# Kernel optimization log

Measured on AMD Instinct MI355X. Metric: run time of the kernel, lower is better.

The kernel has to match this reference:

```python
import jax, jax.numpy as jnp
import numpy as np

B, N, D = 16, 96, 128
NUM_TOKENS, NUM_CLASSES = 14, 10
NUM_ROUNDS = 5


def setup_inputs() -> dict:
    key = jax.random.key(0)
    ks = jax.random.split(key, 8)
    def lin(k, fan_in, shape):
        return (jax.random.normal(k, shape, jnp.float32) / np.sqrt(fan_in)).astype(jnp.float32)
    return {
        "tok": jax.random.randint(ks[0], (B, N), 0, NUM_TOKENS),
        "A": jax.random.uniform(ks[1], (B, N, N), jnp.float32),
        "embed_W": jax.random.normal(ks[2], (NUM_TOKENS, D), jnp.float32),
        "W1": lin(ks[3], 2 * D, (2 * D, D)),   # msg_fc1, stored [in, out]
        "b1": jnp.zeros((D,), jnp.float32),
        "W2": lin(ks[4], D, (D, D)),           # msg_fc2
        "b2": jnp.zeros((D,), jnp.float32),
        "Wo1": lin(ks[5], D, (D, D)),          # out_fc1
        "bo1": jnp.zeros((D,), jnp.float32),
        "Wo2": lin(ks[6], D, (D, NUM_CLASSES)),  # out_fc2 (no bias)
        "alpha": 0, "tau": 1, "beta": 0, "hard": 0,
    }


def reference(tok, A, embed_W, W1, b1, W2, b2, Wo1, bo1, Wo2, alpha, tau, beta, hard):
    # tok: [B,N] int, A: [B,N,N]. Dropout in eval mode (identity).
    e = embed_W[tok]                      # [B,N,D] token embeddings
    centroids = embed_W[4:]               # [10,D]
    W1e, W1x = W1[:D], W1[D:]             # split of msg_fc1 over the concat [e_i ; x_j]
    e_proj = jnp.einsum('bid,de->bie', e, W1e)  # constant across rounds

    def head(x2d):  # out_fc2(relu(out_fc1(x)))
        return jnp.maximum(x2d @ Wo1 + bo1, 0.0) @ Wo2

    def discretize(x):
        logits = head(x.reshape(-1, D))
        # beta=0, hard=False: gumbel_softmax degenerates to tempered softmax
        a = jax.nn.softmax(logits / tau, axis=-1)
        return (a @ centroids).reshape(x.shape)

    x = e
    for r in range(NUM_ROUNDS):
        xj_proj = jnp.einsum('bjd,de->bje', x, W1x)
        # h[b,i,j] = relu(msg_fc1([e_i ; x_j])) without materializing the concat
        h = jnp.maximum(e_proj[:, :, None, :] + xj_proj[:, None, :, :] + b1, 0.0)  # [B,N,N,D]
        m = jnp.maximum(jnp.einsum('bijd,de->bije', h, W2) + b2, 0.0)
        agg = jnp.einsum('bji,bijd->bid', A, m)  # A^T masked sum over j
        x = x + agg
        if r < NUM_ROUNDS - 1:
            # resid=True, alpha=0 -> np.random.random() > 0 a.s. -> residual add
            x = x + discretize(x)
    out = head(x[:, 0, :])                                  # [B,10]
    x_all = head(x.reshape(-1, D)).reshape(B, N, NUM_CLASSES)  # [B,N,10]
    return out, x_all
```

## Files before the change

### kernel.cpp

```cpp
#include <hip/hip_runtime.h>
#include <hip/hip_bf16.h>
#include <math.h>

#define BB   16
#define NN   96
#define DD   128
#define NCLS 10
#define NTOK 14

typedef __attribute__((ext_vector_type(8))) short bf16x8;
typedef __attribute__((ext_vector_type(8))) unsigned short u16x8;
typedef __attribute__((ext_vector_type(4))) float f32x4;

__device__ __forceinline__ float scalar_as_float(int v) {
    if (v >= -1000000 && v <= 1000000) return (float)v;
    return __int_as_float(v);
}
__device__ __forceinline__ unsigned short f2bf(float f) {
    unsigned u = __float_as_uint(f);
    return (unsigned short)((u + 0x7FFFu + ((u >> 16) & 1u)) >> 16);
}
__device__ __forceinline__ unsigned short f2bf_fast(float f) {
    __hip_bfloat16 b = __float2bfloat16(f);
    return *reinterpret_cast<unsigned short*>(&b);
}
__device__ __forceinline__ float bf2f(unsigned short h) {
    return __uint_as_float(((unsigned)h) << 16);
}

#define MFMA(A, B, C) __builtin_amdgcn_mfma_f32_16x16x32_bf16(A, B, C, 0, 0, 0)

__device__ __forceinline__ int swz_bx() {
    const int bxr = blockIdx.x;
    return ((bxr & 7) << 6) | (bxr >> 3);
}

__global__ __launch_bounds__(256) void k_prep(
    const float* __restrict__ A, const float* __restrict__ embed_W,
    const float* __restrict__ W1, const float* __restrict__ b1,
    const float* __restrict__ W2, const float* __restrict__ b2,
    const float* __restrict__ Wo1,
    float* __restrict__ Mtab, float* __restrict__ t2tab, float* __restrict__ AT,
    unsigned short* __restrict__ w2hi, unsigned short* __restrict__ w1xb,
    unsigned short* __restrict__ wo1b)
{
    const int bx = blockIdx.x;
    const int t  = threadIdx.x;
    const float* W1x = W1 + DD * DD;

    if (bx < NTOK * NTOK) {
        const int ti = bx / NTOK, tj = bx % NTOK;
        const int d = t & 127, half = t >> 7;
        __shared__ float part[2][DD];
        __shared__ unsigned short hb[DD];
        {
            const float* erow  = embed_W + (half ? tj : ti) * DD;
            const float* wbase = half ? W1x : W1;
            float acc = 0.f;
#pragma unroll 8
            for (int k = 0; k < DD; ++k)
                acc = fmaf(erow[k], wbase[k * DD + d], acc);
            part[half][d] = acc;
        }
        __syncthreads();
        if (half == 0) {
            const float v = part[0][d] + b1[d];
            if (tj == 0) t2tab[ti * DD + d] = v;
            hb[d] = f2bf(fmaxf(v + part[1][d], 0.f));
        }
        __syncthreads();
        {
            float m = 0.f;
#pragma unroll 8
            for (int kk = 0; kk < 64; ++kk) {
                const int k = half * 64 + kk;
                m = fmaf(bf2f(hb[k]), bf2f(f2bf(W2[k * DD + d])), m);
            }
            part[half][d] = m;
        }
        __syncthreads();
        if (half == 0)
            Mtab[(ti * NTOK + tj) * DD + d] = fmaxf(part[0][d] + part[1][d] + b2[d], 0.f);
    } else if (bx < 212) {
        const int b = bx - 196;
        __shared__ float tile[NN][NN + 1];
        for (int idx = t; idx < NN * NN; idx += 256)
            tile[idx / NN][idx % NN] = A[b * NN * NN + idx];
        __syncthreads();
        for (int idx = t; idx < NN * NN; idx += 256) {
            const int i = idx / NN, j = idx % NN;
            AT[b * NN * NN + idx] = tile[j][i];
        }
    } else if (bx < 220) {
        const int dt = bx - 212;
        const int kc = t >> 6, ll = t & 63;
        const int base = ((dt * 4 + kc) * 64 + ll) * 8;
        const int c = dt * 16 + (ll & 15);
#pragma unroll
        for (int e = 0; e < 8; ++e)
            w2hi[base + e] = f2bf(W2[(kc * 32 + (ll >> 4) * 8 + e) * DD + c]);
    } else if (bx < 224) {
        const int base = (bx - 220) * 4096 + t * 16;
#pragma unroll
        for (int e = 0; e < 16; ++e) w1xb[base + e] = f2bf(W1x[base + e]);
    } else {
        const int base = (bx - 224) * 4096 + t * 16;
#pragma unroll
        for (int e = 0; e < 16; ++e) wo1b[base + e] = f2bf(Wo1[base + e]);
    }
}

__global__ __launch_bounds__(512, 4) void k_round0(
    const int* __restrict__ tok, const float* __restrict__ AT,
    const float* __restrict__ Mtab, const float* __restrict__ embed_W,
    const unsigned short* __restrict__ wo1b, const float* __restrict__ bo1,
    const float* __restrict__ Wo2, const unsigned short* __restrict__ w1xb,
    const int* __restrict__ tau_p,
    float* __restrict__ x, unsigned short* __restrict__ xj_out)
{
    const int bx = swz_bx();
    const int b  = bx >> 5;
    const int is = bx & 31;
    const int t  = threadIdx.x;
    const int w  = t >> 6;
    const int l  = t & 63;
    const int row0 = b * NN + is;

    __shared__ __align__(16) float mt[3][NTOK * DD];
    __shared__ float at3[3][NN];
    __shared__ int   tkj[NN];
    __shared__ float agg_s[3][DD];
    __shared__ float xn_s[3][DD];
    __shared__ float part_s[4][3][DD];

    const int ti0 = tok[row0], ti1 = tok[row0 + 32], ti2 = tok[row0 + 64];
    if (t < NN) {
        tkj[t]    = tok[b * NN + t];
        at3[0][t] = AT[row0 * NN + t];
        at3[1][t] = AT[(row0 + 32) * NN + t];
        at3[2][t] = AT[(row0 + 64) * NN + t];
    }
    for (int idx = t; idx < 3 * NTOK * DD; idx += 512) {
        const int u = idx / (NTOK * DD), rd = idx - u * (NTOK * DD);
        const int tiu = (u == 0) ? ti0 : ((u == 1) ? ti1 : ti2);
        mt[u][rd] = Mtab[tiu * NTOK * DD + rd];
    }
    __syncthreads();

    if (t < 192) {
        const int u = t >> 6, d2 = t & 63;
        const float2* mtu = (const float2*)mt[u];
        float2 acc = {0.f, 0.f};
#pragma unroll 4
        for (int j = 0; j < NN; ++j) {
            const float a = at3[u][j];
            const float2 m = mtu[tkj[j] * 64 + d2];
            acc.x = fmaf(a, m.x, acc.x);
            acc.y = fmaf(a, m.y, acc.y);
        }
        *(float2*)&agg_s[u][d2 * 2] = acc;
    }
    __syncthreads();

    float xr0 = 0.f, xr1 = 0.f;
    if (w < 3) {
        const int tk = (w == 0) ? ti0 : ((w == 1) ? ti1 : ti2);
        xr0 = embed_W[tk * DD + l]      + agg_s[w][l];
        xr1 = embed_W[tk * DD + l + 64] + agg_s[w][l + 64];
        xn_s[w][l]      = xr0;
        xn_s[w][l + 64] = xr1;
    }
    __syncthreads();

    {
        const int q = t >> 7, h = t & 127;
        float p0 = 0.f, p1 = 0.f, p2 = 0.f;
#pragma unroll
        for (int kk = 0; kk < 32; ++kk) {
            const int k = q * 32 + kk;
            const float wv = bf2f(wo1b[k * DD + h]);
            p0 = fmaf(xn_s[0][k], wv, p0);
            p1 = fmaf(xn_s[1][k], wv, p1);
            p2 = fmaf(xn_s[2][k], wv, p2);
        }
        part_s[q][0][h] = p0; part_s[q][1][h] = p1; part_s[q][2][h] = p2;
    }
    __syncthreads();

    if (w < 3) {
        const int row_u = row0 + 32 * w;
        const float hid0 = fmaxf(part_s[0][w][l] + part_s[1][w][l]
                               + part_s[2][w][l] + part_s[3][w][l] + bo1[l], 0.f);
        const float hid1 = fmaxf(part_s[0][w][l + 64] + part_s[1][w][l + 64]
                               + part_s[2][w][l + 64] + part_s[3][w][l + 64] + bo1[l + 64], 0.f);
        float lgp[NCLS];
#pragma unroll
        for (int c = 0; c < NCLS; ++c)
            lgp[c] = hid0 * Wo2[l * NCLS + c] + hid1 * Wo2[(l + 64) * NCLS + c];
#pragma unroll
        for (int s = 1; s < 64; s <<= 1) {
#pragma unroll
            for (int c = 0; c < NCLS; ++c) lgp[c] += __shfl_xor(lgp[c], s);
        }
        float mx = -1e30f;
#pragma unroll
        for (int c = 0; c < NCLS; ++c) mx = fmaxf(mx, lgp[c]);
        const float inv_tau = 1.f / scalar_as_float(tau_p[0]);
        float p[NCLS], den = 0.f;
#pragma unroll
        for (int c = 0; c < NCLS; ++c) { p[c] = expf((lgp[c] - mx) * inv_tau); den += p[c]; }
        const float invden = 1.f / den;
#pragma unroll
        for (int c = 0; c < NCLS; ++c) {
            const float pc = p[c] * invden;
            xr0 = fmaf(pc, embed_W[(4 + c) * DD + l], xr0);
            xr1 = fmaf(pc, embed_W[(4 + c) * DD + l + 64], xr1);
        }
        x[row_u * DD + l]      = xr0;
        x[row_u * DD + l + 64] = xr1;
        xn_s[w][l]      = xr0;
        xn_s[w][l + 64] = xr1;
    }
    __syncthreads();

    {
        const int q = t >> 7, h = t & 127;
        float p0 = 0.f, p1 = 0.f, p2 = 0.f;
#pragma unroll
        for (int kk = 0; kk < 32; ++kk) {
            const int k = q * 32 + kk;
            const float wv = bf2f(w1xb[k * DD + h]);
            p0 = fmaf(xn_s[0][k], wv, p0);
            p1 = fmaf(xn_s[1][k], wv, p1);
            p2 = fmaf(xn_s[2][k], wv, p2);
        }
        part_s[q][0][h] = p0; part_s[q][1][h] = p1; part_s[q][2][h] = p2;
    }
    __syncthreads();

    if (w < 3) {
        const int row_u = row0 + 32 * w;
        xj_out[row_u * DD + l] =
            f2bf_fast(part_s[0][w][l] + part_s[1][w][l] + part_s[2][w][l] + part_s[3][w][l]);
        xj_out[row_u * DD + l + 64] =
            f2bf_fast(part_s[0][w][l + 64] + part_s[1][w][l + 64]
                    + part_s[2][w][l + 64] + part_s[3][w][l + 64]);
    }
}

template<int FIN>
__global__ __launch_bounds__(512, 4) void k_round(
    const int* __restrict__ tok, const float* __restrict__ AT,
    const float* __restrict__ t2tab,
    const unsigned short* __restrict__ xj_in,
    const unsigned short* __restrict__ w2hi, const float* __restrict__ b2,
    const float* __restrict__ Wo1, const unsigned short* __restrict__ wo1b,
    const float* __restrict__ bo1, const float* __restrict__ Wo2,
    const float* __restrict__ embed_W, const unsigned short* __restrict__ w1xb,
    const int* __restrict__ tau_p,
    float* __restrict__ x, unsigned short* __restrict__ xj_out,
    float* __restrict__ out, float* __restrict__ x_all)
{
    const int bx = swz_bx();
    const int b  = bx >> 5;
    const int is = bx & 31;
    const int t  = threadIdx.x;
    const int w  = t >> 6;
    const int l  = t & 63;
    const int jg  = w >> 2;
    const int dg  = w & 3;
    const int jg3 = jg * 3;
    const int d0 = (t & 15) * 8;
    const int row0 = b * NN + is;

    __shared__ __align__(16) unsigned short hs[2][NN * DD];
    __shared__ float ac_s[3][NN];
    __shared__ float agg_part[3][2][DD];
    __shared__ float xn_s[3][DD];
    __shared__ float part_s[4][3][DD];

    const int tk0 = tok[row0], tk1 = tok[row0 + 32], tk2 = tok[row0 + 64];

    if (t < NN) {
        ac_s[0][t] = AT[row0 * NN + t];
        ac_s[1][t] = AT[(row0 + 32) * NN + t];
        ac_s[2][t] = AT[(row0 + 64) * NN + t];
    }
    float xr0 = 0.f, xr1 = 0.f;
    if (w < 3) {
        const int row_u = row0 + 32 * w;
        xr0 = x[row_u * DD + l];
        xr1 = x[row_u * DD + l + 64];
    }

    const bf16x8* WH = (const bf16x8*)w2hi;
    const int f0 = (dg * 4) * 64 + l;
    const int f1 = ((dg + 4) * 4) * 64 + l;
    bf16x8 bh00 = WH[f0],        bh10 = WH[f1];
    bf16x8 bh01 = WH[f0 + 64],   bh11 = WH[f1 + 64];
    bf16x8 bh02 = WH[f0 + 128],  bh12 = WH[f1 + 128];
    bf16x8 bh03 = WH[f0 + 192],  bh13 = WH[f1 + 192];
    asm volatile("" : "+v"(bh00), "+v"(bh01), "+v"(bh02), "+v"(bh03),
                      "+v"(bh10), "+v"(bh11), "+v"(bh12), "+v"(bh13));
    const float b2v0 = b2[dg * 16 + (l & 15)];
    const float b2v1 = b2[64 + dg * 16 + (l & 15)];
    const u16x8* xj8 = (const u16x8*)(xj_in + b * NN * DD);

    const u16x8 xva = xj8[t];
    const u16x8 xvb = xj8[t + 512];
    const u16x8 xvc = xj8[t + 1024];
    const int j_a = t >> 4, j_b = (t + 512) >> 4, j_c = (t + 1024) >> 4;

    auto STAGE = [&](int u, int p) {
        const int tk = (u == 0) ? tk0 : ((u == 1) ? tk1 : tk2);
        const float4 ea = *(const float4*)(t2tab + tk * DD + d0);
        const float4 eb = *(const float4*)(t2tab + tk * DD + d0 + 4);
        float v8[8];
        v8[0] = ea.x; v8[1] = ea.y; v8[2] = ea.z; v8[3] = ea.w;
        v8[4] = eb.x; v8[5] = eb.y; v8[6] = eb.z; v8[7] = eb.w;
        u16x8 hh;
#pragma unroll
        for (int e = 0; e < 8; ++e) hh[e] = f2bf_fast(fmaxf(bf2f(xva[e]) + v8[e], 0.f));
        *(u16x8*)&hs[p][(j_a * DD + d0) ^ ((j_a & 7) << 3)] = hh;
#pragma unroll
        for (int e = 0; e < 8; ++e) hh[e] = f2bf_fast(fmaxf(bf2f(xvb[e]) + v8[e], 0.f));
        *(u16x8*)&hs[p][(j_b * DD + d0) ^ ((j_b & 7) << 3)] = hh;
#pragma unroll
        for (int e = 0; e < 8; ++e) hh[e] = f2bf_fast(fmaxf(bf2f(xvc[e]) + v8[e], 0.f));
        *(u16x8*)&hs[p][(j_c * DD + d0) ^ ((j_c & 7) << 3)] = hh;
    };

    auto GEMM = [&](int u, int p) {
        float aggp0 = 0.f, aggp1 = 0.f;
        const unsigned short* hb = hs[p];
#pragma unroll
        for (int jj = 0; jj < 3; ++jj) {
            const int jt  = jg3 + jj;
            const int r16 = jt * 16 + (l & 15);
            const int ko  = (l >> 4) * 8;
            const int sw  = (r16 & 7) << 3;
            const bf16x8 a0 = *(const bf16x8*)&hb[(r16 * DD + ko     ) ^ sw];
            const bf16x8 a1 = *(const bf16x8*)&hb[(r16 * DD + ko + 32) ^ sw];
            const bf16x8 a2 = *(const bf16x8*)&hb[(r16 * DD + ko + 64) ^ sw];
            const bf16x8 a3 = *(const bf16x8*)&hb[(r16 * DD + ko + 96) ^ sw];
            f32x4 c0 = {0.f, 0.f, 0.f, 0.f}, c1 = {0.f, 0.f, 0.f, 0.f};
            c0 = MFMA(a0, bh00, c0);  c1 = MFMA(a0, bh10, c1);
            c0 = MFMA(a1, bh01, c0);  c1 = MFMA(a1, bh11, c1);
            c0 = MFMA(a2, bh02, c0);  c1 = MFMA(a2, bh12, c1);
            c0 = MFMA(a3, bh03, c0);  c1 = MFMA(a3, bh13, c1);
#pragma unroll
            for (int r = 0; r < 4; ++r) {
                const float a = ac_s[u][jt * 16 + (l >> 4) * 4 + r];
                aggp0 = fmaf(a, fmaxf(c0[r] + b2v0, 0.f), aggp0);
                aggp1 = fmaf(a, fmaxf(c1[r] + b2v1, 0.f), aggp1);
            }
        }
        aggp0 += __shfl_xor(aggp0, 16); aggp0 += __shfl_xor(aggp0, 32);
        aggp1 += __shfl_xor(aggp1, 16); aggp1 += __shfl_xor(aggp1, 32);
        if (l < 16) {
            agg_part[u][jg][dg * 16 + l]      = aggp0;
            agg_part[u][jg][64 + dg * 16 + l] = aggp1;
        }
    };

    STAGE(0, 0);
    __syncthreads();
    STAGE(1, 1);
    GEMM(0, 0);
    __syncthreads();
    STAGE(2, 0);
    GEMM(1, 1);
    __syncthreads();
    GEMM(2, 0);
    __syncthreads();

    if (w < 3) {
        xr0 += agg_part[w][0][l]      + agg_part[w][1][l];
        xr1 += agg_part[w][0][l + 64] + agg_part[w][1][l + 64];
        xn_s[w][l]      = xr0;
        xn_s[w][l + 64] = xr1;
    }
    __syncthreads();

    {
        const int q = t >> 7, h = t & 127;
        float p0 = 0.f, p1 = 0.f, p2 = 0.f;
#pragma unroll
        for (int kk = 0; kk < 32; ++kk) {
            const int k = q * 32 + kk;
            const float wv = FIN ? Wo1[k * DD + h] : bf2f(wo1b[k * DD + h]);
            p0 = fmaf(xn_s[0][k], wv, p0);
            p1 = fmaf(xn_s[1][k], wv, p1);
            p2 = fmaf(xn_s[2][k], wv, p2);
        }
        part_s[q][0][h] = p0; part_s[q][1][h] = p1; part_s[q][2][h] = p2;
    }
    __syncthreads();

    if (w < 3) {
        const int row_u = row0 + 32 * w;
        const float hid0 = fmaxf(part_s[0][w][l] + part_s[1][w][l]
                               + part_s[2][w][l] + part_s[3][w][l] + bo1[l], 0.f);
        const float hid1 = fmaxf(part_s[0][w][l + 64] + part_s[1][w][l + 64]
                               + part_s[2][w][l + 64] + part_s[3][w][l + 64] + bo1[l + 64], 0.f);
        float lgp[NCLS];
#pragma unroll
        for (int c = 0; c < NCLS; ++c)
            lgp[c] = hid0 * Wo2[l * NCLS + c] + hid1 * Wo2[(l + 64) * NCLS + c];
#pragma unroll
        for (int s = 1; s < 64; s <<= 1) {
#pragma unroll
            for (int c = 0; c < NCLS; ++c) lgp[c] += __shfl_xor(lgp[c], s);
        }
        if (FIN) {
#pragma unroll
            for (int c = 0; c < NCLS; ++c) {
                if (l == c) {
                    x_all[row_u * NCLS + c] = lgp[c];
                    if (is == 0 && w == 0) out[b * NCLS + c] = lgp[c];
                }
            }
        } else {
            float mx = -1e30f;
#pragma unroll
            for (int c = 0; c < NCLS; ++c) mx = fmaxf(mx, lgp[c]);
            const float inv_tau = 1.f / scalar_as_float(tau_p[0]);
            float p[NCLS], den = 0.f;
#pragma unroll
            for (int c = 0; c < NCLS; ++c) { p[c] = expf((lgp[c] - mx) * inv_tau); den += p[c]; }
            const float invden = 1.f / den;
#pragma unroll
            for (int c = 0; c < NCLS; ++c) {
                const float pc = p[c] * invden;
                xr0 = fmaf(pc, embed_W[(4 + c) * DD + l], xr0);
                xr1 = fmaf(pc, embed_W[(4 + c) * DD + l + 64], xr1);
            }
            x[row_u * DD + l]      = xr0;
            x[row_u * DD + l + 64] = xr1;
            xn_s[w][l]      = xr0;
            xn_s[w][l + 64] = xr1;
        }
    }
    if (FIN) return;
    __syncthreads();

    {
        const int q = t >> 7, h = t & 127;
        float p0 = 0.f, p1 = 0.f, p2 = 0.f;
#pragma unroll
        for (int kk = 0; kk < 32; ++kk) {
            const int k = q * 32 + kk;
            const float wv = bf2f(w1xb[k * DD + h]);
            p0 = fmaf(xn_s[0][k], wv, p0);
            p1 = fmaf(xn_s[1][k], wv, p1);
            p2 = fmaf(xn_s[2][k], wv, p2);
        }
        part_s[q][0][h] = p0; part_s[q][1][h] = p1; part_s[q][2][h] = p2;
    }
    __syncthreads();

    if (w < 3) {
        const int row_u = row0 + 32 * w;
        xj_out[row_u * DD + l] =
            f2bf_fast(part_s[0][w][l] + part_s[1][w][l] + part_s[2][w][l] + part_s[3][w][l]);
        xj_out[row_u * DD + l + 64] =
            f2bf_fast(part_s[0][w][l + 64] + part_s[1][w][l + 64]
                    + part_s[2][w][l + 64] + part_s[3][w][l + 64]);
    }
}

extern "C" void kernel_launch(void* const* d_in, const int* in_sizes, int n_in,
                              void* d_out, int out_size, void* d_ws, size_t ws_size,
                              hipStream_t stream)
{
    (void)in_sizes; (void)n_in; (void)out_size; (void)ws_size;
    const int*   tok     = (const int*)d_in[0];
    const float* Aab     = (const float*)d_in[1];
    const float* embed_W = (const float*)d_in[2];
    const float* W1      = (const float*)d_in[3];
    const float* b1      = (const float*)d_in[4];
    const float* W2      = (const float*)d_in[5];
    const float* b2      = (const float*)d_in[6];
    const float* Wo1     = (const float*)d_in[7];
    const float* bo1     = (const float*)d_in[8];
    const float* Wo2     = (const float*)d_in[9];
    const int*   tau_p   = (const int*)d_in[11];

    float* out   = (float*)d_out;
    float* x_all = out + BB * NCLS;

    float* ws     = (float*)d_ws;
    float* x      = ws;
    float* ATr    = ws + BB * NN * DD;
    float* Mtab   = ATr + BB * NN * NN;
    float* t2tab  = Mtab + NTOK * NTOK * DD;
    unsigned short* xjA  = (unsigned short*)(t2tab + NTOK * DD);
    unsigned short* xjB  = xjA + BB * NN * DD;
    unsigned short* w2hi = xjB + BB * NN * DD;
    unsigned short* w1xb = w2hi + DD * DD;
    unsigned short* wo1b = w1xb + DD * DD;

    k_prep<<<228, 256, 0, stream>>>(Aab, embed_W, W1, b1, W2, b2, Wo1,
                                    Mtab, t2tab, ATr, w2hi, w1xb, wo1b);
    k_round0<<<512, 512, 0, stream>>>(tok, ATr, Mtab, embed_W, wo1b, bo1,
                                      Wo2, w1xb, tau_p, x, xjA);
    for (int r = 1; r < 5; ++r) {
        const unsigned short* xin = (r & 1) ? xjA : xjB;
        unsigned short*       xot = (r & 1) ? xjB : xjA;
        if (r < 4)
            k_round<0><<<512, 512, 0, stream>>>(tok, ATr, t2tab, xin, w2hi, b2,
                                                Wo1, wo1b, bo1, Wo2, embed_W, w1xb,
                                                tau_p, x, xot, out, x_all);
        else
            k_round<1><<<512, 512, 0, stream>>>(tok, ATr, t2tab, xin, w2hi, b2,
                                                Wo1, wo1b, bo1, Wo2, embed_W, w1xb,
                                                tau_p, x, xot, out, x_all);
    }
}
```

Before: 71.94 us.

## Halve LDS staging buffer and per-wave MFMA tile to raise occupancy

```diff
diff --git a/kernel.cpp b/kernel.cpp
--- a/kernel.cpp
+++ b/kernel.cpp
@@ -249,7 +249,7 @@
 }
 
 template<int FIN>
-__global__ __launch_bounds__(512, 4) void k_round(
+__global__ __launch_bounds__(512, 6) void k_round(
     const int* __restrict__ tok, const float* __restrict__ AT,
     const float* __restrict__ t2tab,
     const unsigned short* __restrict__ xj_in,
@@ -267,15 +267,12 @@
     const int t  = threadIdx.x;
     const int w  = t >> 6;
     const int l  = t & 63;
-    const int jg  = w >> 2;
-    const int dg  = w & 3;
-    const int jg3 = jg * 3;
     const int d0 = (t & 15) * 8;
     const int row0 = b * NN + is;
 
-    __shared__ __align__(16) unsigned short hs[2][NN * DD];
+    __shared__ __align__(16) unsigned short hs[2][48 * DD];
     __shared__ float ac_s[3][NN];
-    __shared__ float agg_part[3][2][DD];
+    __shared__ float agg_part[3][DD];
     __shared__ float xn_s[3][DD];
     __shared__ float part_s[4][3][DD];
 
@@ -294,89 +291,95 @@
     }
 
     const bf16x8* WH = (const bf16x8*)w2hi;
-    const int f0 = (dg * 4) * 64 + l;
-    const int f1 = ((dg + 4) * 4) * 64 + l;
-    bf16x8 bh00 = WH[f0],        bh10 = WH[f1];
-    bf16x8 bh01 = WH[f0 + 64],   bh11 = WH[f1 + 64];
-    bf16x8 bh02 = WH[f0 + 128],  bh12 = WH[f1 + 128];
-    bf16x8 bh03 = WH[f0 + 192],  bh13 = WH[f1 + 192];
-    asm volatile("" : "+v"(bh00), "+v"(bh01), "+v"(bh02), "+v"(bh03),
-                      "+v"(bh10), "+v"(bh11), "+v"(bh12), "+v"(bh13));
-    const float b2v0 = b2[dg * 16 + (l & 15)];
-    const float b2v1 = b2[64 + dg * 16 + (l & 15)];
+    const int f0 = (w * 4) * 64 + l;
+    bf16x8 bh0 = WH[f0];
+    bf16x8 bh1 = WH[f0 + 64];
+    bf16x8 bh2 = WH[f0 + 128];
+    bf16x8 bh3 = WH[f0 + 192];
+    asm volatile("" : "+v"(bh0), "+v"(bh1), "+v"(bh2), "+v"(bh3));
+    const float b2v = b2[w * 16 + (l & 15)];
     const u16x8* xj8 = (const u16x8*)(xj_in + b * NN * DD);
 
-    const u16x8 xva = xj8[t];
-    const u16x8 xvb = xj8[t + 512];
-    const u16x8 xvc = xj8[t + 1024];
-    const int j_a = t >> 4, j_b = (t + 512) >> 4, j_c = (t + 1024) >> 4;
-
-    auto STAGE = [&](int u, int p) {
+    auto STAGE = [&](int u, int jh, int p) {
         const int tk = (u == 0) ? tk0 : ((u == 1) ? tk1 : tk2);
         const float4 ea = *(const float4*)(t2tab + tk * DD + d0);
         const float4 eb = *(const float4*)(t2tab + tk * DD + d0 + 4);
         float v8[8];
         v8[0] = ea.x; v8[1] = ea.y; v8[2] = ea.z; v8[3] = ea.w;
         v8[4] = eb.x; v8[5] = eb.y; v8[6] = eb.z; v8[7] = eb.w;
-        u16x8 hh;
-#pragma unroll
-        for (int e = 0; e < 8; ++e) hh[e] = f2bf_fast(fmaxf(bf2f(xva[e]) + v8[e], 0.f));
-        *(u16x8*)&hs[p][(j_a * DD + d0) ^ ((j_a & 7) << 3)] = hh;
-#pragma unroll
-        for (int e = 0; e < 8; ++e) hh[e] = f2bf_fast(fmaxf(bf2f(xvb[e]) + v8[e], 0.f));
-        *(u16x8*)&hs[p][(j_b * DD + d0) ^ ((j_b & 7) << 3)] = hh;
-#pragma unroll
-        for (int e = 0; e < 8; ++e) hh[e] = f2bf_fast(fmaxf(bf2f(xvc[e]) + v8[e], 0.f));
-        *(u16x8*)&hs[p][(j_c * DD + d0) ^ ((j_c & 7) << 3)] = hh;
+        {
+            const int jl = t >> 4;
+            const u16x8 xv = xj8[(jh * 48 + jl) * 16 + (t & 15)];
+            u16x8 hh;
+#pragma unroll
+            for (int e = 0; e < 8; ++e)
+                hh[e] = f2bf_fast(fmaxf(bf2f(xv[e]) + v8[e], 0.f));
+            *(u16x8*)&hs[p][(jl * DD + d0) ^ ((jl & 7) << 3)] = hh;
+        }
+        if (t < 256) {
+            const int jl = 32 + (t >> 4);
+            const u16x8 xv = xj8[(jh * 48 + jl) * 16 + (t & 15)];
+            u16x8 hh;
+#pragma unroll
+            for (int e = 0; e < 8; ++e)
+                hh[e] = f2bf_fast(fmaxf(bf2f(xv[e]) + v8[e], 0.f));
+            *(u16x8*)&hs[p][(jl * DD + d0) ^ ((jl & 7) << 3)] = hh;
+        }
     };
 
-    auto GEMM = [&](int u, int p) {
-        float aggp0 = 0.f, aggp1 = 0.f;
+    float aggp = 0.f;
+
+    auto GEMM = [&](int u, int jh, int p) {
         const unsigned short* hb = hs[p];
+        const int jb = jh * 48;
 #pragma unroll
         for (int jj = 0; jj < 3; ++jj) {
-            const int jt  = jg3 + jj;
-            const int r16 = jt * 16 + (l & 15);
+            const int r16 = jj * 16 + (l & 15);
             const int ko  = (l >> 4) * 8;
             const int sw  = (r16 & 7) << 3;
             const bf16x8 a0 = *(const bf16x8*)&hb[(r16 * DD + ko     ) ^ sw];
             const bf16x8 a1 = *(const bf16x8*)&hb[(r16 * DD + ko + 32) ^ sw];
             const bf16x8 a2 = *(const bf16x8*)&hb[(r16 * DD + ko + 64) ^ sw];
             const bf16x8 a3 = *(const bf16x8*)&hb[(r16 * DD + ko + 96) ^ sw];
-            f32x4 c0 = {0.f, 0.f, 0.f, 0.f}, c1 = {0.f, 0.f, 0.f, 0.f};
-            c0 = MFMA(a0, bh00, c0);  c1 = MFMA(a0, bh10, c1);
-            c0 = MFMA(a1, bh01, c0);  c1 = MFMA(a1, bh11, c1);
-            c0 = MFMA(a2, bh02, c0);  c1 = MFMA(a2, bh12, c1);
-            c0 = MFMA(a3, bh03, c0);  c1 = MFMA(a3, bh13, c1);
+            f32x4 c0 = {0.f, 0.f, 0.f, 0.f};
+            c0 = MFMA(a0, bh0, c0);
+            c0 = MFMA(a1, bh1, c0);
+            c0 = MFMA(a2, bh2, c0);
+            c0 = MFMA(a3, bh3, c0);
 #pragma unroll
             for (int r = 0; r < 4; ++r) {
-                const float a = ac_s[u][jt * 16 + (l >> 4) * 4 + r];
-                aggp0 = fmaf(a, fmaxf(c0[r] + b2v0, 0.f), aggp0);
-                aggp1 = fmaf(a, fmaxf(c1[r] + b2v1, 0.f), aggp1);
+                const float a = ac_s[u][jb + jj * 16 + (l >> 4) * 4 + r];
+                aggp = fmaf(a, fmaxf(c0[r] + b2v, 0.f), aggp);
             }
         }
-        aggp0 += __shfl_xor(aggp0, 16); aggp0 += __shfl_xor(aggp0, 32);
-        aggp1 += __shfl_xor(aggp1, 16); aggp1 += __shfl_xor(aggp1, 32);
-        if (l < 16) {
-            agg_part[u][jg][dg * 16 + l]      = aggp0;
-            agg_part[u][jg][64 + dg * 16 + l] = aggp1;
-        }
     };
 
-    STAGE(0, 0);
-    __syncthreads();
-    STAGE(1, 1);
-    GEMM(0, 0);
-    __syncthreads();
-    STAGE(2, 0);
-    GEMM(1, 1);
-    __syncthreads();
-    GEMM(2, 0);
-    __syncthreads();
-
-    if (w < 3) {
-        xr0 += agg_part[w][0][l]      + agg_part[w][1][l];
-        xr1 += agg_part[w][0][l + 64] + agg_part[w][1][l + 64];
+    auto FLUSH = [&](int u) {
+        float a = aggp;
+        a += __shfl_xor(a, 16);
+        a += __shfl_xor(a, 32);
+        if (l < 16) agg_part[u][w * 16 + l] = a;
+        aggp = 0.f;
+    };
+
+    STAGE(0, 0, 0);
+    __syncthreads();
+    STAGE(0, 1, 1);  GEMM(0, 0, 0);
+    __syncthreads();
+    STAGE(1, 0, 0);  GEMM(0, 1, 1);  FLUSH(0);
+    __syncthreads();
+    STAGE(1, 1, 1);  GEMM(1, 0, 0);
+    __syncthreads();
+    STAGE(2, 0, 0);  GEMM(1, 1, 1);  FLUSH(1);
+    __syncthreads();
+    STAGE(2, 1, 1);  GEMM(2, 0, 0);
+    __syncthreads();
+    GEMM(2, 1, 1);   FLUSH(2);
+    __syncthreads();
+
+    if (w < 3) {
+        xr0 += agg_part[w][l];
+        xr1 += agg_part[w][l + 64];
         xn_s[w][l]      = xr0;
         xn_s[w][l + 64] = xr1;
     }
```

Result: slower. 97.94 us (+36.1%).
